# Performance work log

Hardware: AMD Instinct MI355X
Metric: run time of the kernel (lower is better)

Reference implementation:

```python
import jax, jax.numpy as jnp
import numpy as np

B, C, NX, NY = 4, 64, 512, 512
N_PER_B = 30000  # non-empty pillars per sample


def setup_inputs() -> dict:
    key = jax.random.key(0)
    voxel_features = jax.random.normal(key, (B * N_PER_B, C), dtype=jnp.float32)
    # Build coords [N,4] = (batch, z, y, x) with unique (x,y) per batch so the
    # scatter-set is deterministic (PointPillars pillar coords are unique).
    rng = np.random.default_rng(0)
    parts = []
    for b in range(B):
        flat = rng.choice(NX * NY, size=N_PER_B, replace=False)
        x = flat // NY
        y = flat % NY
        parts.append(np.stack([np.full(N_PER_B, b, np.int64),
                               np.zeros(N_PER_B, np.int64),
                               y.astype(np.int64),
                               x.astype(np.int64)], axis=1))
    coords = jnp.asarray(np.concatenate(parts, axis=0))
    return {"voxel_features": voxel_features, "coords": coords, "batch_size": B}


def reference(voxel_features, coords, batch_size):
    # Fused single scatter: global flat index = b*nx*ny + x*ny + y
    flat = coords[:, 0] * (NX * NY) + coords[:, 3] * NY + coords[:, 2]  # [N]
    canvas = jnp.zeros((batch_size * NX * NY, C), dtype=voxel_features.dtype)
    canvas = canvas.at[flat].set(voxel_features)  # [B*nx*ny, C]
    # -> [B, C, nx, ny]; reshape (nx, ny) matches index = x*ny + y
    return canvas.reshape(batch_size, NX, NY, C).transpose(0, 3, 1, 2)
```

## Files before the change

### kernel.cpp

```cpp
#include <hip/hip_runtime.h>

#define NXC 512
#define NYC 512
#define CC  64
#define BC  4

__global__ void pp_zero_map(int4* __restrict__ map4, int n4) {
    int i = blockIdx.x * blockDim.x + threadIdx.x;
    if (i < n4) map4[i] = make_int4(0, 0, 0, 0);
}

__global__ void pp_build_map(const int* __restrict__ coords, int* __restrict__ map, int N) {
    int n = blockIdx.x * blockDim.x + threadIdx.x;
    if (n >= N) return;
    int4 c = *(const int4*)(coords + 4 * (size_t)n);
    int b = c.x, y = c.z, x = c.w;
    map[((size_t)b * NXC + x) * NYC + y] = n + 1;
}

__global__ void pp_gather(const float* __restrict__ vf,
                          const int* __restrict__ map,
                          float* __restrict__ out) {
    int bx = blockIdx.x;
    int t  = threadIdx.x;
    int b  = bx >> 9;
    int x  = bx & (NXC - 1);

    int c0 = t >> 7;
    int y4 = (t & 127) << 2;

    int4 nn = *(const int4*)(map + (size_t)bx * NYC + y4);

    const float* v0 = vf + (size_t)(nn.x - 1) * CC;
    const float* v1 = vf + (size_t)(nn.y - 1) * CC;
    const float* v2 = vf + (size_t)(nn.z - 1) * CC;
    const float* v3 = vf + (size_t)(nn.w - 1) * CC;

    float* obase = out + ((size_t)b * CC * NXC + x) * NYC + y4;

    #pragma unroll 4
    for (int c = c0; c < CC; c += 2) {
        float4 v;
        v.x = nn.x ? v0[c] : 0.0f;
        v.y = nn.y ? v1[c] : 0.0f;
        v.z = nn.z ? v2[c] : 0.0f;
        v.w = nn.w ? v3[c] : 0.0f;
        *(float4*)(obase + (size_t)c * (NXC * NYC)) = v;
    }
}

extern "C" void kernel_launch(void* const* d_in, const int* in_sizes, int n_in,
                              void* d_out, int out_size, void* d_ws, size_t ws_size,
                              hipStream_t stream) {
    const float* vf     = (const float*)d_in[0];
    const int*   coords = (const int*)d_in[1];

    float* out = (float*)d_out;
    int*   map = (int*)d_ws;

    const int N = in_sizes[0] / CC;
    const int MAPN  = BC * NXC * NYC;
    const int MAPN4 = MAPN / 4;

    pp_zero_map<<<(MAPN4 + 255) / 256, 256, 0, stream>>>((int4*)map, MAPN4);
    pp_build_map<<<(N + 255) / 256, 256, 0, stream>>>(coords, map, N);
    pp_gather<<<BC * NXC, 256, 0, stream>>>(vf, map, out);
}
```

Before: 324.4 us.

## Remap gather blocks to per-channel x-strips with nontemporal stores

Each gather block now handles one (batch, channel, 64-row x strip) and streams 128 KB of contiguous output, instead of one x row across all channels. The map is reread once per channel (64 times total), but output writes become long contiguous runs. Output stores are marked nontemporal so they bypass cache retention. The cost is heavy map re-reading and scattered single-float feature loads per channel, which may thrash cache compared to the old pattern of row-wise feature reuse.

```diff
diff --git a/kernel.cpp b/kernel.cpp
--- a/kernel.cpp
+++ b/kernel.cpp
@@ -4,6 +4,8 @@
 #define NYC 512
 #define CC  64
 #define BC  4
+
+typedef float v4f __attribute__((ext_vector_type(4)));
 
 __global__ void pp_zero_map(int4* __restrict__ map4, int n4) {
     int i = blockIdx.x * blockDim.x + threadIdx.x;
@@ -14,38 +16,31 @@
     int n = blockIdx.x * blockDim.x + threadIdx.x;
     if (n >= N) return;
     int4 c = *(const int4*)(coords + 4 * (size_t)n);
-    int b = c.x, y = c.z, x = c.w;
-    map[((size_t)b * NXC + x) * NYC + y] = n + 1;
+    map[((size_t)c.x * NXC + c.w) * NYC + c.z] = n + 1;
 }
 
-__global__ void pp_gather(const float* __restrict__ vf,
-                          const int* __restrict__ map,
-                          float* __restrict__ out) {
-    int bx = blockIdx.x;
-    int t  = threadIdx.x;
-    int b  = bx >> 9;
-    int x  = bx & (NXC - 1);
+__global__ void __launch_bounds__(256) pp_gather(const float* __restrict__ vf,
+                                                 const int* __restrict__ map,
+                                                 float* __restrict__ out) {
+    int bid = blockIdx.x;
+    int b   = bid >> 9;
+    int c   = (bid >> 3) & 63;
+    int x0  = (bid & 7) << 6;
+    int t   = threadIdx.x;
 
-    int c0 = t >> 7;
-    int y4 = (t & 127) << 2;
-
-    int4 nn = *(const int4*)(map + (size_t)bx * NYC + y4);
-
-    const float* v0 = vf + (size_t)(nn.x - 1) * CC;
-    const float* v1 = vf + (size_t)(nn.y - 1) * CC;
-    const float* v2 = vf + (size_t)(nn.z - 1) * CC;
-    const float* v3 = vf + (size_t)(nn.w - 1) * CC;
-
-    float* obase = out + ((size_t)b * CC * NXC + x) * NYC + y4;
+    const int* mbase = map + ((size_t)(b * NXC + x0) << 9);
+    float* obase = out + ((size_t)(b * CC + c) * NXC + x0) * NYC;
 
     #pragma unroll 4
-    for (int c = c0; c < CC; c += 2) {
-        float4 v;
-        v.x = nn.x ? v0[c] : 0.0f;
-        v.y = nn.y ? v1[c] : 0.0f;
-        v.z = nn.z ? v2[c] : 0.0f;
-        v.w = nn.w ? v3[c] : 0.0f;
-        *(float4*)(obase + (size_t)c * (NXC * NYC)) = v;
+    for (int i = 0; i < 32; ++i) {
+        int lin = i * 256 + t;
+        int4 m = *(const int4*)(mbase + 4 * (size_t)lin);
+        v4f v;
+        v.x = m.x ? vf[(size_t)(m.x - 1) * CC + c] : 0.0f;
+        v.y = m.y ? vf[(size_t)(m.y - 1) * CC + c] : 0.0f;
+        v.z = m.z ? vf[(size_t)(m.z - 1) * CC + c] : 0.0f;
+        v.w = m.w ? vf[(size_t)(m.w - 1) * CC + c] : 0.0f;
+        __builtin_nontemporal_store(v, (v4f*)(obase + 4 * (size_t)lin));
     }
 }
 
@@ -64,5 +59,5 @@
 
     pp_zero_map<<<(MAPN4 + 255) / 256, 256, 0, stream>>>((int4*)map, MAPN4);
     pp_build_map<<<(N + 255) / 256, 256, 0, stream>>>(coords, map, N);
-    pp_gather<<<BC * NXC, 256, 0, stream>>>(vf, map, out);
+    pp_gather<<<BC * CC * 8, 256, 0, stream>>>(vf, map, out);
 }
```

New measurement: 353.9 us. 9.1% more time.
